# Optimization experiments

Hardware: AMD Instinct MI355X
Metric: run time of the kernel (lower is better)

Reference implementation:

```python
import jax, jax.numpy as jnp
import numpy as np

N_NODES = 100000
N_EDGES = 1000000
DIM = 64


def rel_graph_conv(x, src, dst, etype, W, Ws, b, act):
    # DGL RelGraphConv (regularizer=None, self_loop=True, bias=True, sum agg):
    # out_i = act( sum_{(j->i)} W_{r} x_j + x_i @ Ws + b )
    # num_rels=2: transform once per relation, then select per edge.
    h = jnp.einsum('nd,rdo->rno', x, W)              # [2, N, out]
    m = jnp.where((etype == 0)[:, None], h[0][src], h[1][src])  # [E, out]
    agg = jax.ops.segment_sum(m, dst, num_segments=x.shape[0])  # [N, out]
    out = agg + x @ Ws + b
    return act(out) if act is not None else out


def setup_inputs() -> dict:
    key = jax.random.key(0)
    ks = jax.random.split(key, 16)
    scale = 1.0 / np.sqrt(DIM)
    inp = {
        'features': jax.random.normal(ks[0], (N_NODES, DIM), dtype=jnp.float32),
        'src': jax.random.randint(ks[1], (N_EDGES,), 0, N_NODES, dtype=jnp.int32),
        'dst': jax.random.randint(ks[2], (N_EDGES,), 0, N_NODES, dtype=jnp.int32),
        'etype': jax.random.randint(ks[3], (N_EDGES,), 0, 2, dtype=jnp.int32),
    }
    for i in range(3):
        inp[f'W{i}'] = jax.random.normal(ks[4 + 3 * i], (2, DIM, DIM), dtype=jnp.float32) * scale
        inp[f'Ws{i}'] = jax.random.normal(ks[5 + 3 * i], (DIM, DIM), dtype=jnp.float32) * scale
        inp[f'b{i}'] = jnp.zeros((DIM,), dtype=jnp.float32)
    return inp


def reference(features, src, dst, etype, W0, Ws0, b0, W1, Ws1, b1, W2, Ws2, b2):
    # dropout is identity in eval mode
    h = rel_graph_conv(features, src, dst, etype, W0, Ws0, b0, jax.nn.relu)
    h = rel_graph_conv(h, src, dst, etype, W1, Ws1, b1, jax.nn.relu)
    h = rel_graph_conv(h, src, dst, etype, W2, Ws2, b2, None)
    return h
```

## Files before the change

### kernel.cpp

```cpp
#include <hip/hip_runtime.h>

#define NN 100000
#define NE 1000000
#define NEP (NE + 6 * NN)
#define DIM 64
#define ZPITCH 200
#define SCHUNK 1024
#define SBLOCKS ((NN + SCHUNK - 1) / SCHUNK)
#define PAD4(c) (((c) + 3) & ~3)
#define NPART 8

typedef __attribute__((ext_vector_type(8))) short short8;
typedef __attribute__((ext_vector_type(4))) float f32x4;
typedef __attribute__((ext_vector_type(4))) _Float16 h4;
typedef __attribute__((ext_vector_type(8))) _Float16 h8;

union HU { uint2 u; h4 h; };

__device__ __forceinline__ ushort f2h(float f) {
    union { _Float16 h; ushort u; } c; c.h = (_Float16)f; return c.u;
}

__global__ __launch_bounds__(256) void zero_buf(int* p, int len) {
    int i = blockIdx.x * 256 + threadIdx.x;
    if (i < len) p[i] = 0;
}

__global__ __launch_bounds__(256) void count_rank2p(const int* __restrict__ dst,
                                                    const int* __restrict__ et,
                                                    int* __restrict__ cnt2p,
                                                    int* __restrict__ rank) {
    int e = blockIdx.x * 256 + threadIdx.x;
    int p = blockIdx.x & (NPART - 1);
    if (e < NE) rank[e] = atomicAdd(&cnt2p[p * 2 * NN + dst[e] * 2 + et[e]], 1);
}

__global__ __launch_bounds__(256) void merge_counts(int* __restrict__ cnt2p,
                                                    int* __restrict__ cnt2) {
    int i = blockIdx.x * 256 + threadIdx.x;
    if (i < 2 * NN) {
        int s = 0;
#pragma unroll
        for (int p = 0; p < NPART; ++p) {
            int v = cnt2p[p * 2 * NN + i];
            cnt2p[p * 2 * NN + i] = s;
            s += v;
        }
        cnt2[i] = s;
    }
}

__global__ __launch_bounds__(256) void scan_partial2p(const int* __restrict__ cnt2,
                                                      int* __restrict__ bsum) {
    int t = threadIdx.x, lane = t & 63, wid = t >> 6;
    int base = blockIdx.x * SCHUNK + t * 4;
    int s = 0;
#pragma unroll
    for (int k = 0; k < 4; ++k) {
        int i = base + k;
        if (i < NN) s += PAD4(cnt2[2 * i]) + PAD4(cnt2[2 * i + 1]);
    }
#pragma unroll
    for (int off = 32; off > 0; off >>= 1) s += __shfl_down(s, off, 64);
    __shared__ int wtot[4];
    if (lane == 0) wtot[wid] = s;
    __syncthreads();
    if (t == 0) bsum[blockIdx.x] = wtot[0] + wtot[1] + wtot[2] + wtot[3];
}

__global__ __launch_bounds__(128) void scan_bsums(const int* __restrict__ bsum,
                                                  int* __restrict__ bsum_ex) {
    __shared__ int sh[128];
    int t = threadIdx.x;
    int v = (t < SBLOCKS) ? bsum[t] : 0;
    sh[t] = v;
    __syncthreads();
    for (int off = 1; off < 128; off <<= 1) {
        int u = (t >= off) ? sh[t - off] : 0;
        __syncthreads();
        sh[t] += u;
        __syncthreads();
    }
    if (t < SBLOCKS) bsum_ex[t] = sh[t] - v;
}

__global__ __launch_bounds__(256) void scan_final2p(const int* __restrict__ cnt2,
                                                    const int* __restrict__ bsum_ex,
                                                    int* __restrict__ row_ptr) {
    int t = threadIdx.x, lane = t & 63, wid = t >> 6;
    int base = blockIdx.x * SCHUNK + t * 4;
    int c[4];
#pragma unroll
    for (int k = 0; k < 4; ++k) {
        int i = base + k;
        c[k] = (i < NN) ? (PAD4(cnt2[2 * i]) + PAD4(cnt2[2 * i + 1])) : 0;
    }
    int s = c[0] + c[1] + c[2] + c[3];
    int incl = s;
#pragma unroll
    for (int off = 1; off < 64; off <<= 1) {
        int u = __shfl_up(incl, off, 64);
        if (lane >= off) incl += u;
    }
    __shared__ int wtot[4];
    if (lane == 63) wtot[wid] = incl;
    __syncthreads();
    int woff = 0;
    for (int w = 0; w < wid; ++w) woff += wtot[w];
    int run = bsum_ex[blockIdx.x] + woff + (incl - s);
#pragma unroll
    for (int k = 0; k < 4; ++k) {
        int i = base + k;
        if (i < NN) row_ptr[i] = run;
        run += c[k];
    }
}

__global__ __launch_bounds__(256) void pad_fill(const int* __restrict__ row_ptr,
                                                const int* __restrict__ cnt2,
                                                int* __restrict__ esrc) {
    int i = blockIdx.x * 256 + threadIdx.x;
    if (i < 2 * NN) {
        int n = i >> 1, r = i & 1;
        int2 c = *(const int2*)(cnt2 + 2 * n);
        int cr = r ? c.y : c.x;
        int base = row_ptr[n] + (r ? PAD4(c.x) : 0) + cr;
        int np = PAD4(cr) - cr;
        for (int k = 0; k < np; ++k) esrc[base + k] = NN;
    } else if (i < 2 * NN + 4) {
        esrc[NEP + (i - 2 * NN)] = NN;
    }
}

__global__ __launch_bounds__(256) void fill_edges4p(const int* __restrict__ src,
                                                    const int* __restrict__ dst,
                                                    const int* __restrict__ et,
                                                    const int* __restrict__ rank,
                                                    const int* __restrict__ row_ptr,
                                                    const int* __restrict__ cnt2,
                                                    const int* __restrict__ cnt2p,
                                                    int* __restrict__ esrc) {
    int e = blockIdx.x * 256 + threadIdx.x;
    int p = blockIdx.x & (NPART - 1);
    if (e < NE) {
        int d = dst[e], r = et[e];
        int pre = cnt2p[p * 2 * NN + 2 * d + r];
        int pos = row_ptr[d] + pre + rank[e] + (r ? PAD4(cnt2[2 * d]) : 0);
        esrc[pos] = src[e];
    }
}

__global__ __launch_bounds__(256) void convert_feat(const float* __restrict__ x,
                                                    ushort* __restrict__ xb,
                                                    ushort* __restrict__ xb1) {
    int b = blockIdx.x;
    if (b == NN * 16 / 256) {
        int t = threadIdx.x;
        if (t < 64) {
            xb[(size_t)NN * DIM + t] = 0;
            xb1[(size_t)NN * DIM + t] = 0;
        }
        return;
    }
    int i = b * 256 + threadIdx.x;
    float4 v = ((const float4*)x)[i];
    union { ushort u[4]; uint2 w; } o;
    o.u[0] = f2h(v.x); o.u[1] = f2h(v.y); o.u[2] = f2h(v.z); o.u[3] = f2h(v.w);
    *(uint2*)(xb + (size_t)i * 4) = o.w;
}

__global__ __launch_bounds__(256) void prep_w_all(
    const float* __restrict__ W0, const float* __restrict__ Ws0,
    const float* __restrict__ W1, const float* __restrict__ Ws1,
    const float* __restrict__ W2, const float* __restrict__ Ws2,
    ushort* __restrict__ wt) {
    int idx = blockIdx.x * 256 + threadIdx.x;
    int l = idx / 12288, rr = idx % 12288;
    const float* W  = (l == 0) ? W0 : (l == 1) ? W1 : W2;
    const float* Ws = (l == 0) ? Ws0 : (l == 1) ? Ws1 : Ws2;
    int k = rr >> 6, n = rr & 63;
    float v = (k < 128) ? W[k * 64 + n] : Ws[(k - 128) * 64 + n];
    wt[l * 12288 + n * 192 + k] = f2h(v);
}

__global__ __launch_bounds__(256) void rgcn_aggregate_g(
    const uint2* __restrict__ xb2, const int* __restrict__ row_ptr,
    const int* __restrict__ cnt2, const int* __restrict__ esrc,
    uint2* __restrict__ agg2)
{
    int t = threadIdx.x, lane = t & 63, wid = t >> 6;
    int g = lane >> 4, s = lane & 15;
    int n = blockIdx.x * 16 + wid * 4 + g;
    int start = row_ptr[n];
    int2 c = *(const int2*)(cnt2 + 2 * n);
    int c0p = PAD4(c.x), c1p = PAD4(c.y);
    int tmax = c0p > c1p ? c0p : c1p;
    int b1 = start + c0p;

    const uint2* xrow = xb2 + s;
    HU z; z.u.x = 0u; z.u.y = 0u;
    h4 a0 = z.h, a1 = z.h;

    for (int j = 0; j < tmax; j += 4) {
        int i0 = (j < c0p) ? start + j : NEP;
        int i1 = (j < c1p) ? b1 + j : NEP;
        int4 qa = *(const int4*)(esrc + i0);
        int4 qb = *(const int4*)(esrc + i1);
        HU w0, w1, w2, w3, w4, w5, w6, w7;
        w0.u = xrow[(size_t)qa.x * 16];
        w1.u = xrow[(size_t)qa.y * 16];
        w2.u = xrow[(size_t)qa.z * 16];
        w3.u = xrow[(size_t)qa.w * 16];
        w4.u = xrow[(size_t)qb.x * 16];
        w5.u = xrow[(size_t)qb.y * 16];
        w6.u = xrow[(size_t)qb.z * 16];
        w7.u = xrow[(size_t)qb.w * 16];
        a0 += w0.h; a0 += w1.h; a0 += w2.h; a0 += w3.h;
        a1 += w4.h; a1 += w5.h; a1 += w6.h; a1 += w7.h;
    }

    HU o0, o1; o0.h = a0; o1.h = a1;
    agg2[(size_t)n * 32 + s] = o0.u;
    agg2[(size_t)n * 32 + 16 + s] = o1.u;
}

__global__ __launch_bounds__(256) void rgcn_transform_mfma(
    const ushort* __restrict__ agg,
    const ushort* __restrict__ xb,
    const ushort* __restrict__ wt,
    const float* __restrict__ bias,
    float* __restrict__ outf,
    ushort* __restrict__ xbn,
    int mode)
{
    __shared__ ushort sZ[64 * ZPITCH];

    int t = threadIdx.x, lane = t & 63, wid = t >> 6;
    int quad = lane >> 4, l16 = lane & 15;

    h8 bh[6];
    {
        const ushort* wh = wt + (size_t)(wid * 16 + l16) * 192;
#pragma unroll
        for (int kk = 0; kk < 6; ++kk)
            bh[kk] = *(const h8*)(wh + kk * 32 + quad * 8);
    }
    float bv = bias[wid * 16 + l16];

    int n0 = blockIdx.x * 64;
    for (int i = t; i < 1024; i += 256) {
        int node = i >> 4, c8 = i & 15;
        int n = n0 + node;
        uint4 v = {0u, 0u, 0u, 0u};
        if (n < NN) v = *(const uint4*)(agg + (size_t)n * 128 + c8 * 8);
        *(uint4*)(sZ + node * ZPITCH + c8 * 8) = v;
    }
    for (int i = t; i < 512; i += 256) {
        int node = i >> 3, c8 = i & 7;
        int n = n0 + node;
        uint4 v = {0u, 0u, 0u, 0u};
        if (n < NN) v = *(const uint4*)(xb + (size_t)n * DIM + c8 * 8);
        *(uint4*)(sZ + node * ZPITCH + 128 + c8 * 8) = v;
    }
    __syncthreads();

    f32x4 acc[4];
#pragma unroll
    for (int mt = 0; mt < 4; ++mt) acc[mt] = (f32x4){bv, bv, bv, bv};

#pragma unroll
    for (int kk = 0; kk < 6; ++kk) {
#pragma unroll
        for (int mt = 0; mt < 4; ++mt) {
            h8 a = *(const h8*)(sZ + (mt * 16 + l16) * ZPITCH + kk * 32 + quad * 8);
            acc[mt] = __builtin_amdgcn_mfma_f32_16x16x32_f16(a, bh[kk], acc[mt], 0, 0, 0);
        }
    }

    int col = wid * 16 + l16;
#pragma unroll
    for (int mt = 0; mt < 4; ++mt) {
#pragma unroll
        for (int r = 0; r < 4; ++r) {
            int node = n0 + mt * 16 + quad * 4 + r;
            if (node < NN) {
                float v = acc[mt][r];
                if (mode) outf[(size_t)node * DIM + col] = v;
                else      xbn[(size_t)node * DIM + col] = f2h(fmaxf(v, 0.f));
            }
        }
    }
}

extern "C" void kernel_launch(void* const* d_in, const int* in_sizes, int n_in,
                              void* d_out, int out_size, void* d_ws, size_t ws_size,
                              hipStream_t stream)
{
    const float* feat = (const float*)d_in[0];
    const int*   src  = (const int*)d_in[1];
    const int*   dst  = (const int*)d_in[2];
    const int*   et   = (const int*)d_in[3];
    const float* W[3]  = { (const float*)d_in[4], (const float*)d_in[7], (const float*)d_in[10] };
    const float* Ws[3] = { (const float*)d_in[5], (const float*)d_in[8], (const float*)d_in[11] };
    const float* b[3]  = { (const float*)d_in[6], (const float*)d_in[9], (const float*)d_in[12] };

    uint*   agg   = (uint*)d_ws;
    ushort* xbuf0 = (ushort*)(agg + (size_t)NN * 64);
    ushort* xbuf1 = xbuf0 + (size_t)(NN + 1) * DIM;
    ushort* wt    = xbuf1 + (size_t)(NN + 1) * DIM;
    int* esrc    = (int*)(wt + 3 * 12288);
    int* rank    = esrc + NEP + 4;
    int* cnt2    = rank + NE;
    int* cnt2p   = cnt2 + 2 * NN;
    int* row_ptr = cnt2p + NPART * 2 * NN;
    int* bsum    = row_ptr + NN;
    int* bsum_ex = bsum + SBLOCKS;
    float* outF  = (float*)d_out;

    const dim3 tb(256);
    const int zgrid = (NPART * 2 * NN + 255) / 256;
    const int egrid = (NE + 255) / 256;
    const int mgrid = (2 * NN + 255) / 256;
    const int pgrid = (2 * NN + 4 + 255) / 256;
    const int tgrid = (NN + 63) / 64;
    const int agrid = NN / 16;

    zero_buf<<<zgrid, tb, 0, stream>>>(cnt2p, NPART * 2 * NN);
    count_rank2p<<<egrid, tb, 0, stream>>>(dst, et, cnt2p, rank);
    merge_counts<<<mgrid, tb, 0, stream>>>(cnt2p, cnt2);
    scan_partial2p<<<SBLOCKS, tb, 0, stream>>>(cnt2, bsum);
    scan_bsums<<<1, 128, 0, stream>>>(bsum, bsum_ex);
    scan_final2p<<<SBLOCKS, tb, 0, stream>>>(cnt2, bsum_ex, row_ptr);
    pad_fill<<<pgrid, tb, 0, stream>>>(row_ptr, cnt2, esrc);
    fill_edges4p<<<egrid, tb, 0, stream>>>(src, dst, et, rank, row_ptr, cnt2, cnt2p, esrc);

    prep_w_all<<<144, tb, 0, stream>>>(W[0], Ws[0], W[1], Ws[1], W[2], Ws[2], wt);
    convert_feat<<<NN * 16 / 256 + 1, tb, 0, stream>>>(feat, xbuf0, xbuf1);

    rgcn_aggregate_g<<<agrid, tb, 0, stream>>>((const uint2*)xbuf0, row_ptr, cnt2, esrc, (uint2*)agg);
    rgcn_transform_mfma<<<tgrid, tb, 0, stream>>>((const ushort*)agg, xbuf0, wt, b[0], nullptr, xbuf1, 0);
    rgcn_aggregate_g<<<agrid, tb, 0, stream>>>((const uint2*)xbuf1, row_ptr, cnt2, esrc, (uint2*)agg);
    rgcn_transform_mfma<<<tgrid, tb, 0, stream>>>((const ushort*)agg, xbuf1, wt + 12288, b[1], nullptr, xbuf0, 0);
    rgcn_aggregate_g<<<agrid, tb, 0, stream>>>((const uint2*)xbuf0, row_ptr, cnt2, esrc, (uint2*)agg);
    rgcn_transform_mfma<<<tgrid, tb, 0, stream>>>((const ushort*)agg, xbuf0, wt + 2 * 12288, b[2], outF, nullptr, 1);
}
```

Baseline: 301.6 us.

## Fuse edge aggregation into MFMA transform kernel via shared memory

Merges the gather-aggregate kernel and the MFMA transform kernel into one kernel per layer. Each block aggregates its 64 nodes' per-relation neighbor sums directly into shared memory, then runs the MFMA matmul with the self-loop features. This removes the global agg buffer round-trip and three launches. In exchange, each block's gather phase now processes 4 nodes per 16-lane group sequentially, which lowers parallelism and memory-level parallelism per block.

```diff
diff --git a/kernel.cpp b/kernel.cpp
--- a/kernel.cpp
+++ b/kernel.cpp
@@ -183,50 +183,12 @@
     wt[l * 12288 + n * 192 + k] = f2h(v);
 }
 
-__global__ __launch_bounds__(256) void rgcn_aggregate_g(
-    const uint2* __restrict__ xb2, const int* __restrict__ row_ptr,
-    const int* __restrict__ cnt2, const int* __restrict__ esrc,
-    uint2* __restrict__ agg2)
-{
-    int t = threadIdx.x, lane = t & 63, wid = t >> 6;
-    int g = lane >> 4, s = lane & 15;
-    int n = blockIdx.x * 16 + wid * 4 + g;
-    int start = row_ptr[n];
-    int2 c = *(const int2*)(cnt2 + 2 * n);
-    int c0p = PAD4(c.x), c1p = PAD4(c.y);
-    int tmax = c0p > c1p ? c0p : c1p;
-    int b1 = start + c0p;
-
-    const uint2* xrow = xb2 + s;
-    HU z; z.u.x = 0u; z.u.y = 0u;
-    h4 a0 = z.h, a1 = z.h;
-
-    for (int j = 0; j < tmax; j += 4) {
-        int i0 = (j < c0p) ? start + j : NEP;
-        int i1 = (j < c1p) ? b1 + j : NEP;
-        int4 qa = *(const int4*)(esrc + i0);
-        int4 qb = *(const int4*)(esrc + i1);
-        HU w0, w1, w2, w3, w4, w5, w6, w7;
-        w0.u = xrow[(size_t)qa.x * 16];
-        w1.u = xrow[(size_t)qa.y * 16];
-        w2.u = xrow[(size_t)qa.z * 16];
-        w3.u = xrow[(size_t)qa.w * 16];
-        w4.u = xrow[(size_t)qb.x * 16];
-        w5.u = xrow[(size_t)qb.y * 16];
-        w6.u = xrow[(size_t)qb.z * 16];
-        w7.u = xrow[(size_t)qb.w * 16];
-        a0 += w0.h; a0 += w1.h; a0 += w2.h; a0 += w3.h;
-        a1 += w4.h; a1 += w5.h; a1 += w6.h; a1 += w7.h;
-    }
-
-    HU o0, o1; o0.h = a0; o1.h = a1;
-    agg2[(size_t)n * 32 + s] = o0.u;
-    agg2[(size_t)n * 32 + 16 + s] = o1.u;
-}
-
-__global__ __launch_bounds__(256) void rgcn_transform_mfma(
-    const ushort* __restrict__ agg,
+__global__ __launch_bounds__(256) void rgcn_fused(
+    const uint2* __restrict__ xb2,
     const ushort* __restrict__ xb,
+    const int* __restrict__ row_ptr,
+    const int* __restrict__ cnt2,
+    const int* __restrict__ esrc,
     const ushort* __restrict__ wt,
     const float* __restrict__ bias,
     float* __restrict__ outf,
@@ -237,6 +199,7 @@
 
     int t = threadIdx.x, lane = t & 63, wid = t >> 6;
     int quad = lane >> 4, l16 = lane & 15;
+    int n0 = blockIdx.x * 64;
 
     h8 bh[6];
     {
@@ -247,20 +210,58 @@
     }
     float bv = bias[wid * 16 + l16];
 
-    int n0 = blockIdx.x * 64;
-    for (int i = t; i < 1024; i += 256) {
-        int node = i >> 4, c8 = i & 15;
-        int n = n0 + node;
-        uint4 v = {0u, 0u, 0u, 0u};
-        if (n < NN) v = *(const uint4*)(agg + (size_t)n * 128 + c8 * 8);
-        *(uint4*)(sZ + node * ZPITCH + c8 * 8) = v;
-    }
-    for (int i = t; i < 512; i += 256) {
+    uint4 xv[2];
+#pragma unroll
+    for (int r = 0; r < 2; ++r) {
+        int i = t + r * 256;
         int node = i >> 3, c8 = i & 7;
         int n = n0 + node;
         uint4 v = {0u, 0u, 0u, 0u};
         if (n < NN) v = *(const uint4*)(xb + (size_t)n * DIM + c8 * 8);
-        *(uint4*)(sZ + node * ZPITCH + 128 + c8 * 8) = v;
+        xv[r] = v;
+    }
+
+    int gi = wid * 4 + quad, s = l16;
+    const uint2* xrow = xb2 + s;
+    for (int k = 0; k < 4; ++k) {
+        int nl = gi * 4 + k;
+        int n = n0 + nl;
+        HU z; z.u.x = 0u; z.u.y = 0u;
+        h4 a0 = z.h, a1 = z.h;
+        if (n < NN) {
+            int start = row_ptr[n];
+            int2 c = *(const int2*)(cnt2 + 2 * n);
+            int c0p = PAD4(c.x), c1p = PAD4(c.y);
+            int tmax = c0p > c1p ? c0p : c1p;
+            int b1 = start + c0p;
+            for (int j = 0; j < tmax; j += 4) {
+                int i0 = (j < c0p) ? start + j : NEP;
+                int i1 = (j < c1p) ? b1 + j : NEP;
+                int4 qa = *(const int4*)(esrc + i0);
+                int4 qb = *(const int4*)(esrc + i1);
+                HU w0, w1, w2, w3, w4, w5, w6, w7;
+                w0.u = xrow[(size_t)qa.x * 16];
+                w1.u = xrow[(size_t)qa.y * 16];
+                w2.u = xrow[(size_t)qa.z * 16];
+                w3.u = xrow[(size_t)qa.w * 16];
+                w4.u = xrow[(size_t)qb.x * 16];
+                w5.u = xrow[(size_t)qb.y * 16];
+                w6.u = xrow[(size_t)qb.z * 16];
+                w7.u = xrow[(size_t)qb.w * 16];
+                a0 += w0.h; a0 += w1.h; a0 += w2.h; a0 += w3.h;
+                a1 += w4.h; a1 += w5.h; a1 += w6.h; a1 += w7.h;
+            }
+        }
+        HU o0, o1; o0.h = a0; o1.h = a1;
+        *(uint2*)(sZ + nl * ZPITCH + 4 * s) = o0.u;
+        *(uint2*)(sZ + nl * ZPITCH + 64 + 4 * s) = o1.u;
+    }
+
+#pragma unroll
+    for (int r = 0; r < 2; ++r) {
+        int i = t + r * 256;
+        int node = i >> 3, c8 = i & 7;
+        *(uint4*)(sZ + node * ZPITCH + 128 + c8 * 8) = xv[r];
     }
     __syncthreads();
 
@@ -304,8 +305,7 @@
     const float* Ws[3] = { (const float*)d_in[5], (const float*)d_in[8], (const float*)d_in[11] };
     const float* b[3]  = { (const float*)d_in[6], (const float*)d_in[9], (const float*)d_in[12] };
 
-    uint*   agg   = (uint*)d_ws;
-    ushort* xbuf0 = (ushort*)(agg + (size_t)NN * 64);
+    ushort* xbuf0 = (ushort*)d_ws;
     ushort* xbuf1 = xbuf0 + (size_t)(NN + 1) * DIM;
     ushort* wt    = xbuf1 + (size_t)(NN + 1) * DIM;
     int* esrc    = (int*)(wt + 3 * 12288);
@@ -323,7 +323,6 @@
     const int mgrid = (2 * NN + 255) / 256;
     const int pgrid = (2 * NN + 4 + 255) / 256;
     const int tgrid = (NN + 63) / 64;
-    const int agrid = NN / 16;
 
     zero_buf<<<zgrid, tb, 0, stream>>>(cnt2p, NPART * 2 * NN);
     count_rank2p<<<egrid, tb, 0, stream>>>(dst, et, cnt2p, rank);
@@ -337,10 +336,10 @@
     prep_w_all<<<144, tb, 0, stream>>>(W[0], Ws[0], W[1], Ws[1], W[2], Ws[2], wt);
     convert_feat<<<NN * 16 / 256 + 1, tb, 0, stream>>>(feat, xbuf0, xbuf1);
 
-    rgcn_aggregate_g<<<agrid, tb, 0, stream>>>((const uint2*)xbuf0, row_ptr, cnt2, esrc, (uint2*)agg);
-    rgcn_transform_mfma<<<tgrid, tb, 0, stream>>>((const ushort*)agg, xbuf0, wt, b[0], nullptr, xbuf1, 0);
-    rgcn_aggregate_g<<<agrid, tb, 0, stream>>>((const uint2*)xbuf1, row_ptr, cnt2, esrc, (uint2*)agg);
-    rgcn_transform_mfma<<<tgrid, tb, 0, stream>>>((const ushort*)agg, xbuf1, wt + 12288, b[1], nullptr, xbuf0, 0);
-    rgcn_aggregate_g<<<agrid, tb, 0, stream>>>((const uint2*)xbuf0, row_ptr, cnt2, esrc, (uint2*)agg);
-    rgcn_transform_mfma<<<tgrid, tb, 0, stream>>>((const ushort*)agg, xbuf0, wt + 2 * 12288, b[2], outF, nullptr, 1);
-}
+    rgcn_fused<<<tgrid, tb, 0, stream>>>((const uint2*)xbuf0, xbuf0, row_ptr, cnt2, esrc,
+                                         wt, b[0], nullptr, xbuf1, 0);
+    rgcn_fused<<<tgrid, tb, 0, stream>>>((const uint2*)xbuf1, xbuf1, row_ptr, cnt2, esrc,
+                                         wt + 12288, b[1], nullptr, xbuf0, 0);
+    rgcn_fused<<<tgrid, tb, 0, stream>>>((const uint2*)xbuf0, xbuf0, row_ptr, cnt2, esrc,
+                                         wt + 2 * 12288, b[2], outF, nullptr, 1);
+}
```

Result: no change. 303.5 us (+0.6%).

## Drop per-edge rank array and aggregate two nodes per lane group

Applied to the files above, without the earlier changes.

The CSR build no longer stores a per-edge rank from the counting pass. The fill pass instead takes the slot with a second atomicAdd on the per-partition prefix counters, which removes a 4 MB write and read. The aggregation kernel now has each 16-lane group handle two destination nodes at once, issuing 16 independent gathers per iteration to raise memory-level parallelism. The cost is a bigger loop-trip imbalance, since the loop runs to the max padded degree of both nodes, plus higher register pressure and half as many blocks.

```diff
diff --git a/kernel.cpp b/kernel.cpp
--- a/kernel.cpp
+++ b/kernel.cpp
@@ -26,13 +26,12 @@
     if (i < len) p[i] = 0;
 }
 
-__global__ __launch_bounds__(256) void count_rank2p(const int* __restrict__ dst,
-                                                    const int* __restrict__ et,
-                                                    int* __restrict__ cnt2p,
-                                                    int* __restrict__ rank) {
+__global__ __launch_bounds__(256) void count2p(const int* __restrict__ dst,
+                                               const int* __restrict__ et,
+                                               int* __restrict__ cnt2p) {
     int e = blockIdx.x * 256 + threadIdx.x;
     int p = blockIdx.x & (NPART - 1);
-    if (e < NE) rank[e] = atomicAdd(&cnt2p[p * 2 * NN + dst[e] * 2 + et[e]], 1);
+    if (e < NE) atomicAdd(&cnt2p[p * 2 * NN + dst[e] * 2 + et[e]], 1);
 }
 
 __global__ __launch_bounds__(256) void merge_counts(int* __restrict__ cnt2p,
@@ -135,17 +134,16 @@
 __global__ __launch_bounds__(256) void fill_edges4p(const int* __restrict__ src,
                                                     const int* __restrict__ dst,
                                                     const int* __restrict__ et,
-                                                    const int* __restrict__ rank,
                                                     const int* __restrict__ row_ptr,
                                                     const int* __restrict__ cnt2,
-                                                    const int* __restrict__ cnt2p,
+                                                    int* __restrict__ cnt2p,
                                                     int* __restrict__ esrc) {
     int e = blockIdx.x * 256 + threadIdx.x;
     int p = blockIdx.x & (NPART - 1);
     if (e < NE) {
         int d = dst[e], r = et[e];
-        int pre = cnt2p[p * 2 * NN + 2 * d + r];
-        int pos = row_ptr[d] + pre + rank[e] + (r ? PAD4(cnt2[2 * d]) : 0);
+        int loc = atomicAdd(&cnt2p[p * 2 * NN + 2 * d + r], 1);
+        int pos = row_ptr[d] + loc + (r ? PAD4(cnt2[2 * d]) : 0);
         esrc[pos] = src[e];
     }
 }
@@ -183,45 +181,68 @@
     wt[l * 12288 + n * 192 + k] = f2h(v);
 }
 
-__global__ __launch_bounds__(256) void rgcn_aggregate_g(
+__global__ __launch_bounds__(256) void rgcn_aggregate_g2(
     const uint2* __restrict__ xb2, const int* __restrict__ row_ptr,
     const int* __restrict__ cnt2, const int* __restrict__ esrc,
     uint2* __restrict__ agg2)
 {
     int t = threadIdx.x, lane = t & 63, wid = t >> 6;
     int g = lane >> 4, s = lane & 15;
-    int n = blockIdx.x * 16 + wid * 4 + g;
-    int start = row_ptr[n];
-    int2 c = *(const int2*)(cnt2 + 2 * n);
-    int c0p = PAD4(c.x), c1p = PAD4(c.y);
-    int tmax = c0p > c1p ? c0p : c1p;
-    int b1 = start + c0p;
+    int gi = wid * 4 + g;
+    int nA = blockIdx.x * 32 + gi * 2;
+    int nB = nA + 1;
+
+    int sA = row_ptr[nA], sB = row_ptr[nB];
+    int2 cA = *(const int2*)(cnt2 + 2 * nA);
+    int2 cB = *(const int2*)(cnt2 + 2 * nB);
+    int a0p = PAD4(cA.x), a1p = PAD4(cA.y);
+    int b0p = PAD4(cB.x), b1p = PAD4(cB.y);
+    int baseA1 = sA + a0p, baseB1 = sB + b0p;
+    int m0 = a0p > a1p ? a0p : a1p;
+    int m1 = b0p > b1p ? b0p : b1p;
+    int tmax = m0 > m1 ? m0 : m1;
 
     const uint2* xrow = xb2 + s;
     HU z; z.u.x = 0u; z.u.y = 0u;
-    h4 a0 = z.h, a1 = z.h;
+    h4 aa0 = z.h, aa1 = z.h, ba0 = z.h, ba1 = z.h;
 
     for (int j = 0; j < tmax; j += 4) {
-        int i0 = (j < c0p) ? start + j : NEP;
-        int i1 = (j < c1p) ? b1 + j : NEP;
-        int4 qa = *(const int4*)(esrc + i0);
-        int4 qb = *(const int4*)(esrc + i1);
-        HU w0, w1, w2, w3, w4, w5, w6, w7;
-        w0.u = xrow[(size_t)qa.x * 16];
-        w1.u = xrow[(size_t)qa.y * 16];
-        w2.u = xrow[(size_t)qa.z * 16];
-        w3.u = xrow[(size_t)qa.w * 16];
-        w4.u = xrow[(size_t)qb.x * 16];
-        w5.u = xrow[(size_t)qb.y * 16];
-        w6.u = xrow[(size_t)qb.z * 16];
-        w7.u = xrow[(size_t)qb.w * 16];
-        a0 += w0.h; a0 += w1.h; a0 += w2.h; a0 += w3.h;
-        a1 += w4.h; a1 += w5.h; a1 += w6.h; a1 += w7.h;
-    }
-
-    HU o0, o1; o0.h = a0; o1.h = a1;
-    agg2[(size_t)n * 32 + s] = o0.u;
-    agg2[(size_t)n * 32 + 16 + s] = o1.u;
+        int i0 = (j < a0p) ? sA + j : NEP;
+        int i1 = (j < a1p) ? baseA1 + j : NEP;
+        int i2 = (j < b0p) ? sB + j : NEP;
+        int i3 = (j < b1p) ? baseB1 + j : NEP;
+        int4 q0 = *(const int4*)(esrc + i0);
+        int4 q1 = *(const int4*)(esrc + i1);
+        int4 q2 = *(const int4*)(esrc + i2);
+        int4 q3 = *(const int4*)(esrc + i3);
+        HU w0, w1, w2, w3, w4, w5, w6, w7, w8, w9, wa, wb, wc, wd, we, wf;
+        w0.u = xrow[(size_t)q0.x * 16];
+        w1.u = xrow[(size_t)q0.y * 16];
+        w2.u = xrow[(size_t)q0.z * 16];
+        w3.u = xrow[(size_t)q0.w * 16];
+        w4.u = xrow[(size_t)q1.x * 16];
+        w5.u = xrow[(size_t)q1.y * 16];
+        w6.u = xrow[(size_t)q1.z * 16];
+        w7.u = xrow[(size_t)q1.w * 16];
+        w8.u = xrow[(size_t)q2.x * 16];
+        w9.u = xrow[(size_t)q2.y * 16];
+        wa.u = xrow[(size_t)q2.z * 16];
+        wb.u = xrow[(size_t)q2.w * 16];
+        wc.u = xrow[(size_t)q3.x * 16];
+        wd.u = xrow[(size_t)q3.y * 16];
+        we.u = xrow[(size_t)q3.z * 16];
+        wf.u = xrow[(size_t)q3.w * 16];
+        aa0 += w0.h; aa0 += w1.h; aa0 += w2.h; aa0 += w3.h;
+        aa1 += w4.h; aa1 += w5.h; aa1 += w6.h; aa1 += w7.h;
+        ba0 += w8.h; ba0 += w9.h; ba0 += wa.h; ba0 += wb.h;
+        ba1 += wc.h; ba1 += wd.h; ba1 += we.h; ba1 += wf.h;
+    }
+
+    HU o;
+    o.h = aa0; agg2[(size_t)nA * 32 + s] = o.u;
+    o.h = aa1; agg2[(size_t)nA * 32 + 16 + s] = o.u;
+    o.h = ba0; agg2[(size_t)nB * 32 + s] = o.u;
+    o.h = ba1; agg2[(size_t)nB * 32 + 16 + s] = o.u;
 }
 
 __global__ __launch_bounds__(256) void rgcn_transform_mfma(
@@ -309,8 +330,7 @@
     ushort* xbuf1 = xbuf0 + (size_t)(NN + 1) * DIM;
     ushort* wt    = xbuf1 + (size_t)(NN + 1) * DIM;
     int* esrc    = (int*)(wt + 3 * 12288);
-    int* rank    = esrc + NEP + 4;
-    int* cnt2    = rank + NE;
+    int* cnt2    = esrc + NEP + 4;
     int* cnt2p   = cnt2 + 2 * NN;
     int* row_ptr = cnt2p + NPART * 2 * NN;
     int* bsum    = row_ptr + NN;
@@ -323,24 +343,24 @@
     const int mgrid = (2 * NN + 255) / 256;
     const int pgrid = (2 * NN + 4 + 255) / 256;
     const int tgrid = (NN + 63) / 64;
-    const int agrid = NN / 16;
+    const int agrid = NN / 32;
 
     zero_buf<<<zgrid, tb, 0, stream>>>(cnt2p, NPART * 2 * NN);
-    count_rank2p<<<egrid, tb, 0, stream>>>(dst, et, cnt2p, rank);
+    count2p<<<egrid, tb, 0, stream>>>(dst, et, cnt2p);
     merge_counts<<<mgrid, tb, 0, stream>>>(cnt2p, cnt2);
     scan_partial2p<<<SBLOCKS, tb, 0, stream>>>(cnt2, bsum);
     scan_bsums<<<1, 128, 0, stream>>>(bsum, bsum_ex);
     scan_final2p<<<SBLOCKS, tb, 0, stream>>>(cnt2, bsum_ex, row_ptr);
     pad_fill<<<pgrid, tb, 0, stream>>>(row_ptr, cnt2, esrc);
-    fill_edges4p<<<egrid, tb, 0, stream>>>(src, dst, et, rank, row_ptr, cnt2, cnt2p, esrc);
+    fill_edges4p<<<egrid, tb, 0, stream>>>(src, dst, et, row_ptr, cnt2, cnt2p, esrc);
 
     prep_w_all<<<144, tb, 0, stream>>>(W[0], Ws[0], W[1], Ws[1], W[2], Ws[2], wt);
     convert_feat<<<NN * 16 / 256 + 1, tb, 0, stream>>>(feat, xbuf0, xbuf1);
 
-    rgcn_aggregate_g<<<agrid, tb, 0, stream>>>((const uint2*)xbuf0, row_ptr, cnt2, esrc, (uint2*)agg);
+    rgcn_aggregate_g2<<<agrid, tb, 0, stream>>>((const uint2*)xbuf0, row_ptr, cnt2, esrc, (uint2*)agg);
     rgcn_transform_mfma<<<tgrid, tb, 0, stream>>>((const ushort*)agg, xbuf0, wt, b[0], nullptr, xbuf1, 0);
-    rgcn_aggregate_g<<<agrid, tb, 0, stream>>>((const uint2*)xbuf1, row_ptr, cnt2, esrc, (uint2*)agg);
+    rgcn_aggregate_g2<<<agrid, tb, 0, stream>>>((const uint2*)xbuf1, row_ptr, cnt2, esrc, (uint2*)agg);
     rgcn_transform_mfma<<<tgrid, tb, 0, stream>>>((const ushort*)agg, xbuf1, wt + 12288, b[1], nullptr, xbuf0, 0);
-    rgcn_aggregate_g<<<agrid, tb, 0, stream>>>((const uint2*)xbuf0, row_ptr, cnt2, esrc, (uint2*)agg);
+    rgcn_aggregate_g2<<<agrid, tb, 0, stream>>>((const uint2*)xbuf0, row_ptr, cnt2, esrc, (uint2*)agg);
     rgcn_transform_mfma<<<tgrid, tb, 0, stream>>>((const ushort*)agg, xbuf0, wt + 2 * 12288, b[2], outF, nullptr, 1);
 }
```

Result: slower. 335.7 us (+11.3%).
